# Performance work log

Hardware: AMD Instinct MI355X
Metric: run time of the kernel (lower is better)

The kernel has to match this reference:

```python
import jax, jax.numpy as jnp
import numpy as np

N_NODES = 50000
N_EDGES = 20000
EDGE_SIZE = 32
IN_CH = 256
OUT_CH = 256


def setup_inputs() -> dict:
    key = jax.random.key(0)
    k1, k2, k3 = jax.random.split(key, 3)
    x = jax.random.normal(k1, (N_NODES, IN_CH), dtype=jnp.float32)
    hyperedges = jax.random.randint(k2, (N_EDGES, EDGE_SIZE), 0, N_NODES)
    weight = jax.random.normal(k3, (IN_CH, OUT_CH), dtype=jnp.float32)
    return {"x": x, "hyperedges": hyperedges, "weight": weight}


def reference(x, hyperedges, weight):
    # Gather node features per hyperedge and reduce ('sum' aggregation):
    # [E, K, C] -> [E, C]
    edge_sum = x[hyperedges].sum(axis=1)
    # Scatter-add each hyperedge's summed feature back to every member node.
    agg = jnp.zeros_like(x).at[hyperedges].add(edge_sum[:, None, :])
    # Dense projection + ReLU.
    return jax.nn.relu(agg @ weight)
```

## Files before the change

### kernel.cpp

```cpp
#include <hip/hip_runtime.h>
#include <hip/hip_bf16.h>
#include <hip/hip_fp16.h>

#define N_NODES 50000
#define N_EDGES 20000
#define EDGE_K  32
#define CH      256
#define N_INC   (N_EDGES * EDGE_K)
#define ELL_CAP 64
#define NSLICE  8
#define SCH     32
#define ZROW    N_EDGES

typedef __attribute__((ext_vector_type(4))) float f32x4;
typedef __attribute__((ext_vector_type(8))) _Float16 f16x8;

static __device__ __forceinline__ __half2 u2h2(unsigned int u) {
    __half2 h; __builtin_memcpy(&h, &u, 4); return h;
}
static __device__ __forceinline__ unsigned int h22u(__half2 h) {
    unsigned int u; __builtin_memcpy(&u, &h, 4); return u;
}
static __device__ __forceinline__ unsigned int pk2h(float a, float b) {
    return h22u(__halves2half2(__float2half_rn(a), __float2half_rn(b)));
}

#define CONV_BLOCKS (N_NODES * CH / 8 / 256)
#define ZERO_BLOCKS ((N_NODES + 255) / 256)
#define ELLI_BLOCKS (N_NODES * ELL_CAP / 2 / 256)
__global__ void prep_kernel(const float* __restrict__ x, unsigned short* __restrict__ xb,
                            const float* __restrict__ w, unsigned short* __restrict__ wt,
                            int* __restrict__ deg, unsigned int* __restrict__ ellu,
                            unsigned short* __restrict__ yb) {
    int b = blockIdx.x;
    if (b < CONV_BLOCKS) {
        int i = b * 256 + threadIdx.x;
        int n = i >> 5, sub = i & 31;
        int g = sub >> 2, cp = (sub & 3) * 8;
        const float* src = x + (size_t)n * CH + sub * 8;
        f32x4 v0 = *reinterpret_cast<const f32x4*>(src);
        f32x4 v1 = *reinterpret_cast<const f32x4*>(src + 4);
        uint4 u;
        u.x = pk2h(v0.x, v0.y);
        u.y = pk2h(v0.z, v0.w);
        u.z = pk2h(v1.x, v1.y);
        u.w = pk2h(v1.z, v1.w);
        *reinterpret_cast<uint4*>(xb + ((size_t)g * N_NODES + n) * SCH + cp) = u;
    } else if (b < CONV_BLOCKS + CH) {
        int n = b - CONV_BLOCKS;
        int k = threadIdx.x;
        __half h = __float2half_rn(w[k * CH + n]);
        wt[n * CH + k] = *reinterpret_cast<unsigned short*>(&h);
    } else if (b < CONV_BLOCKS + CH + ZERO_BLOCKS) {
        int i = (b - CONV_BLOCKS - CH) * 256 + threadIdx.x;
        if (i < N_NODES) deg[i] = 0;
    } else if (b < CONV_BLOCKS + CH + ZERO_BLOCKS + ELLI_BLOCKS) {
        int i = (b - CONV_BLOCKS - CH - ZERO_BLOCKS) * 256 + threadIdx.x;
        ellu[i] = 0x4E204E20u;
    } else {
        int g = threadIdx.x >> 5, c = threadIdx.x & 31;
        yb[((size_t)g * (N_EDGES + 1) + ZROW) * SCH + c] = 0;
    }
}

#define FILL_GROUPS   8
#define NODES_PER_GRP (N_NODES / FILL_GROUPS)
#define FILL_WIN      2560
#define FILL_BLOCKS   ((N_INC / FILL_WIN) * FILL_GROUPS)
#define GGRP          (N_EDGES / 16)
#define GATHER_BLOCKS (GGRP * NSLICE)
__global__ __launch_bounds__(256, 4) void gather_fill_kernel(
        const unsigned short* __restrict__ xb, const int* __restrict__ he,
        unsigned short* __restrict__ es, int* __restrict__ deg,
        unsigned short* __restrict__ ell) {
    int b = blockIdx.x;
    if (b < FILL_BLOCKS) {
        int g  = b % FILL_GROUPS;
        int wn = b / FILL_GROUPS;
        int lo = g * NODES_PER_GRP, hi = lo + NODES_PER_GRP;
        int base = wn * FILL_WIN;
#pragma unroll
        for (int it = 0; it < FILL_WIN / 256; ++it) {
            int i = base + it * 256 + threadIdx.x;
            int node = he[i];
            if (node >= lo && node < hi) {
                int slot = atomicAdd(&deg[node], 1);
                if (slot < ELL_CAP)
                    ell[(size_t)node * ELL_CAP + slot] = (unsigned short)(i >> 5);
            }
        }
        return;
    }
    int gb  = b - FILL_BLOCKS;
    int g   = gb & 7;
    int grp = gb >> 3;
    int w = threadIdx.x >> 6, lane = threadIdx.x & 63;
    int ebase = grp * 16 + w * 4;
    const int* hp = he + (size_t)ebase * EDGE_K;
    int s = lane & 15;
    int ep = lane >> 4, k = (lane >> 2) & 3, q = lane & 3;
    int mA = hp[ep * 32 + s];
    int mB = hp[ep * 32 + 16 + s];
    const unsigned short* xg = xb + (size_t)g * N_NODES * SCH;
    int hb = lane & 48;
    int e0 = __shfl(mA, hb + ((0 + k) & 15), 64);
    int e1 = __shfl(mA, hb + ((4 + k) & 15), 64);
    int e2 = __shfl(mA, hb + ((8 + k) & 15), 64);
    int e3 = __shfl(mA, hb + ((12 + k) & 15), 64);
    int e4 = __shfl(mB, hb + ((0 + k) & 15), 64);
    int e5 = __shfl(mB, hb + ((4 + k) & 15), 64);
    int e6 = __shfl(mB, hb + ((8 + k) & 15), 64);
    int e7 = __shfl(mB, hb + ((12 + k) & 15), 64);
    uint4 d0 = *reinterpret_cast<const uint4*>(xg + (size_t)e0 * SCH + q * 8);
    uint4 d1 = *reinterpret_cast<const uint4*>(xg + (size_t)e1 * SCH + q * 8);
    uint4 d2 = *reinterpret_cast<const uint4*>(xg + (size_t)e2 * SCH + q * 8);
    uint4 d3 = *reinterpret_cast<const uint4*>(xg + (size_t)e3 * SCH + q * 8);
    uint4 d4 = *reinterpret_cast<const uint4*>(xg + (size_t)e4 * SCH + q * 8);
    uint4 d5 = *reinterpret_cast<const uint4*>(xg + (size_t)e5 * SCH + q * 8);
    uint4 d6 = *reinterpret_cast<const uint4*>(xg + (size_t)e6 * SCH + q * 8);
    uint4 d7 = *reinterpret_cast<const uint4*>(xg + (size_t)e7 * SCH + q * 8);
    __half2 a0 = u2h2(0u), a1 = u2h2(0u), a2 = u2h2(0u), a3 = u2h2(0u);
    a0 = __hadd2(a0, u2h2(d0.x)); a1 = __hadd2(a1, u2h2(d0.y));
    a2 = __hadd2(a2, u2h2(d0.z)); a3 = __hadd2(a3, u2h2(d0.w));
    a0 = __hadd2(a0, u2h2(d1.x)); a1 = __hadd2(a1, u2h2(d1.y));
    a2 = __hadd2(a2, u2h2(d1.z)); a3 = __hadd2(a3, u2h2(d1.w));
    a0 = __hadd2(a0, u2h2(d2.x)); a1 = __hadd2(a1, u2h2(d2.y));
    a2 = __hadd2(a2, u2h2(d2.z)); a3 = __hadd2(a3, u2h2(d2.w));
    a0 = __hadd2(a0, u2h2(d3.x)); a1 = __hadd2(a1, u2h2(d3.y));
    a2 = __hadd2(a2, u2h2(d3.z)); a3 = __hadd2(a3, u2h2(d3.w));
    a0 = __hadd2(a0, u2h2(d4.x)); a1 = __hadd2(a1, u2h2(d4.y));
    a2 = __hadd2(a2, u2h2(d4.z)); a3 = __hadd2(a3, u2h2(d4.w));
    a0 = __hadd2(a0, u2h2(d5.x)); a1 = __hadd2(a1, u2h2(d5.y));
    a2 = __hadd2(a2, u2h2(d5.z)); a3 = __hadd2(a3, u2h2(d5.w));
    a0 = __hadd2(a0, u2h2(d6.x)); a1 = __hadd2(a1, u2h2(d6.y));
    a2 = __hadd2(a2, u2h2(d6.z)); a3 = __hadd2(a3, u2h2(d6.w));
    a0 = __hadd2(a0, u2h2(d7.x)); a1 = __hadd2(a1, u2h2(d7.y));
    a2 = __hadd2(a2, u2h2(d7.z)); a3 = __hadd2(a3, u2h2(d7.w));
    a0 = __hadd2(a0, u2h2(__shfl_xor(h22u(a0), 4, 64)));
    a1 = __hadd2(a1, u2h2(__shfl_xor(h22u(a1), 4, 64)));
    a2 = __hadd2(a2, u2h2(__shfl_xor(h22u(a2), 4, 64)));
    a3 = __hadd2(a3, u2h2(__shfl_xor(h22u(a3), 4, 64)));
    a0 = __hadd2(a0, u2h2(__shfl_xor(h22u(a0), 8, 64)));
    a1 = __hadd2(a1, u2h2(__shfl_xor(h22u(a1), 8, 64)));
    a2 = __hadd2(a2, u2h2(__shfl_xor(h22u(a2), 8, 64)));
    a3 = __hadd2(a3, u2h2(__shfl_xor(h22u(a3), 8, 64)));
    if ((lane & 12) == 0) {
        uint4 u;
        u.x = h22u(a0); u.y = h22u(a1); u.z = h22u(a2); u.w = h22u(a3);
        *reinterpret_cast<uint4*>(es + (size_t)(ebase + ep) * CH + g * SCH + q * 8) = u;
    }
}

__global__ __launch_bounds__(256) void gemm_kernel(const unsigned short* __restrict__ es,
                                                   const unsigned short* __restrict__ wt,
                                                   unsigned short* __restrict__ yb) {
    int wid  = threadIdx.x >> 6;
    int lane = threadIdx.x & 63;
    int m0   = blockIdx.x * 64 + wid * 16;
    if (m0 >= N_EDGES) return;
    int lr = lane & 15;
    int lg = lane >> 4;

    f32x4 acc[16] = {};
    const unsigned short* arow = es + (size_t)(m0 + lr) * CH + lg * 8;
#pragma unroll
    for (int kk = 0; kk < CH; kk += 32) {
        f16x8 a = *reinterpret_cast<const f16x8*>(arow + kk);
#pragma unroll
        for (int nt = 0; nt < 16; ++nt) {
            f16x8 bb = *reinterpret_cast<const f16x8*>(
                wt + (size_t)(nt * 16 + lr) * CH + kk + lg * 8);
            acc[nt] = __builtin_amdgcn_mfma_f32_16x16x32_f16(a, bb, acc[nt], 0, 0, 0);
        }
    }
#pragma unroll
    for (int nt = 0; nt < 16; ++nt) {
#pragma unroll
        for (int r = 0; r < 4; ++r) {
            int row = m0 + lg * 4 + r;
            __half h = __float2half_rn(acc[nt][r]);
            yb[((size_t)(nt >> 1) * (N_EDGES + 1) + row) * SCH + (nt & 1) * 16 + lr] =
                *reinterpret_cast<unsigned short*>(&h);
        }
    }
}

#define AP_NPB    16
#define AP_BLOCKS ((N_NODES / AP_NPB) * NSLICE)
__global__ __launch_bounds__(256) void apply_kernel(
        const unsigned short* __restrict__ yb, const int* __restrict__ deg,
        const unsigned short* __restrict__ ell, float* __restrict__ out) {
    int b = blockIdx.x;
    int g = b & 7;
    int w = threadIdx.x >> 6, lane = threadIdx.x & 63;
    int np = lane >> 4, s = lane & 15, k = (lane >> 2) & 3, q = lane & 3;
    int node = (b >> 3) * AP_NPB + w * 4 + np;
    int d = deg[node];
    if (d > ELL_CAP) d = ELL_CAP;
    const unsigned short* er = ell + (size_t)node * ELL_CAP;
    int m0 = er[s], m1 = er[16 + s], m2 = er[32 + s], m3 = er[48 + s];
    int dmax = d;
    dmax = max(dmax, __shfl_xor(dmax, 16, 64));
    dmax = max(dmax, __shfl_xor(dmax, 32, 64));
    const unsigned short* yg = yb + (size_t)g * (N_EDGES + 1) * SCH;
    int hb = lane & 48;
    __half2 a0 = u2h2(0u), a1 = u2h2(0u), a2 = u2h2(0u), a3 = u2h2(0u);
    for (int rq = 0; rq < 4; ++rq) {
        if (rq * 16 >= dmax) break;
        int m = (rq == 0) ? m0 : (rq == 1) ? m1 : (rq == 2) ? m2 : m3;
        int e0 = __shfl(m, hb + 0 + k, 64);
        int e1 = __shfl(m, hb + 4 + k, 64);
        int e2 = __shfl(m, hb + 8 + k, 64);
        int e3 = __shfl(m, hb + 12 + k, 64);
        uint4 d0 = *reinterpret_cast<const uint4*>(yg + (size_t)e0 * SCH + q * 8);
        uint4 d1 = *reinterpret_cast<const uint4*>(yg + (size_t)e1 * SCH + q * 8);
        uint4 d2 = *reinterpret_cast<const uint4*>(yg + (size_t)e2 * SCH + q * 8);
        uint4 d3 = *reinterpret_cast<const uint4*>(yg + (size_t)e3 * SCH + q * 8);
        a0 = __hadd2(a0, u2h2(d0.x)); a1 = __hadd2(a1, u2h2(d0.y));
        a2 = __hadd2(a2, u2h2(d0.z)); a3 = __hadd2(a3, u2h2(d0.w));
        a0 = __hadd2(a0, u2h2(d1.x)); a1 = __hadd2(a1, u2h2(d1.y));
        a2 = __hadd2(a2, u2h2(d1.z)); a3 = __hadd2(a3, u2h2(d1.w));
        a0 = __hadd2(a0, u2h2(d2.x)); a1 = __hadd2(a1, u2h2(d2.y));
        a2 = __hadd2(a2, u2h2(d2.z)); a3 = __hadd2(a3, u2h2(d2.w));
        a0 = __hadd2(a0, u2h2(d3.x)); a1 = __hadd2(a1, u2h2(d3.y));
        a2 = __hadd2(a2, u2h2(d3.z)); a3 = __hadd2(a3, u2h2(d3.w));
    }
    a0 = __hadd2(a0, u2h2(__shfl_xor(h22u(a0), 4, 64)));
    a1 = __hadd2(a1, u2h2(__shfl_xor(h22u(a1), 4, 64)));
    a2 = __hadd2(a2, u2h2(__shfl_xor(h22u(a2), 4, 64)));
    a3 = __hadd2(a3, u2h2(__shfl_xor(h22u(a3), 4, 64)));
    a0 = __hadd2(a0, u2h2(__shfl_xor(h22u(a0), 8, 64)));
    a1 = __hadd2(a1, u2h2(__shfl_xor(h22u(a1), 8, 64)));
    a2 = __hadd2(a2, u2h2(__shfl_xor(h22u(a2), 8, 64)));
    a3 = __hadd2(a3, u2h2(__shfl_xor(h22u(a3), 8, 64)));
    if ((lane & 12) == 0) {
        float2 f0 = __half22float2(a0);
        float2 f1 = __half22float2(a1);
        float2 f2 = __half22float2(a2);
        float2 f3 = __half22float2(a3);
        f32x4 r0, r1;
        r0.x = fmaxf(f0.x, 0.f); r0.y = fmaxf(f0.y, 0.f);
        r0.z = fmaxf(f1.x, 0.f); r0.w = fmaxf(f1.y, 0.f);
        r1.x = fmaxf(f2.x, 0.f); r1.y = fmaxf(f2.y, 0.f);
        r1.z = fmaxf(f3.x, 0.f); r1.w = fmaxf(f3.y, 0.f);
        float* dst = out + (size_t)node * CH + g * SCH + q * 8;
        *reinterpret_cast<f32x4*>(dst)     = r0;
        *reinterpret_cast<f32x4*>(dst + 4) = r1;
    }
}

extern "C" void kernel_launch(void* const* d_in, const int* in_sizes, int n_in,
                              void* d_out, int out_size, void* d_ws, size_t ws_size,
                              hipStream_t stream) {
    const float* x  = (const float*)d_in[0];
    const int*   he = (const int*)d_in[1];
    const float* w  = (const float*)d_in[2];
    float* out = (float*)d_out;

    char* ws = (char*)d_ws;
    unsigned short* wt  = (unsigned short*)ws;
    unsigned short* es  = (unsigned short*)(ws + 131072);
    unsigned short* yb  = (unsigned short*)(ws + 10371072);
    int* deg = (int*)(ws + 20611584);
    unsigned short* ell = (unsigned short*)(ws + 20811584);

    unsigned short* xb = (unsigned short*)d_out;

    prep_kernel<<<CONV_BLOCKS + CH + ZERO_BLOCKS + ELLI_BLOCKS + 1, 256, 0, stream>>>(
        x, xb, w, wt, deg, (unsigned int*)ell, yb);

    gather_fill_kernel<<<FILL_BLOCKS + GATHER_BLOCKS, 256, 0, stream>>>(xb, he, es, deg, ell);

    {
        int blocks = (N_EDGES + 63) / 64;
        gemm_kernel<<<blocks, 256, 0, stream>>>(es, wt, yb);
    }

    apply_kernel<<<AP_BLOCKS, 256, 0, stream>>>(yb, deg, ell, out);
}
```

Baseline: 140.9 us.

## Move ELL fill into prep kernel, drop ELL init, unroll apply gather loads

Moves the hyperedge-to-node ELL fill from the gather kernel into the prep kernel and replaces the in-kernel degree zeroing with a memset. The ELL sentinel initialisation is dropped; the apply kernel now masks slots past the node degree to the zero row. The apply kernel issues 8 gather loads up front (16 when needed) instead of a 4-wide loop, and gets a launch bound of 4 blocks per CU. The aim is to cut ELL-init memory traffic, overlap fill atomics with the fp16 conversion, and raise memory-level parallelism in the apply step. This adds one extra memset launch.

```diff
diff --git a/kernel.cpp b/kernel.cpp
--- a/kernel.cpp
+++ b/kernel.cpp
@@ -25,16 +25,33 @@
     return h22u(__halves2half2(__float2half_rn(a), __float2half_rn(b)));
 }
 
-#define CONV_BLOCKS (N_NODES * CH / 8 / 256)
-#define ZERO_BLOCKS ((N_NODES + 255) / 256)
-#define ELLI_BLOCKS (N_NODES * ELL_CAP / 2 / 256)
+#define FILL_GROUPS   8
+#define NODES_PER_GRP (N_NODES / FILL_GROUPS)
+#define FILL_WIN      2560
+#define FILL_BLOCKS   ((N_INC / FILL_WIN) * FILL_GROUPS)
+#define CONV_BLOCKS   (N_NODES * CH / 8 / 256)
 __global__ void prep_kernel(const float* __restrict__ x, unsigned short* __restrict__ xb,
                             const float* __restrict__ w, unsigned short* __restrict__ wt,
-                            int* __restrict__ deg, unsigned int* __restrict__ ellu,
-                            unsigned short* __restrict__ yb) {
+                            const int* __restrict__ he, int* __restrict__ deg,
+                            unsigned short* __restrict__ ell, unsigned short* __restrict__ yb) {
     int b = blockIdx.x;
-    if (b < CONV_BLOCKS) {
-        int i = b * 256 + threadIdx.x;
+    if (b < FILL_BLOCKS) {
+        int g  = b % FILL_GROUPS;
+        int wn = b / FILL_GROUPS;
+        int lo = g * NODES_PER_GRP, hi = lo + NODES_PER_GRP;
+        int base = wn * FILL_WIN;
+#pragma unroll
+        for (int it = 0; it < FILL_WIN / 256; ++it) {
+            int i = base + it * 256 + threadIdx.x;
+            int node = he[i];
+            if (node >= lo && node < hi) {
+                int slot = atomicAdd(&deg[node], 1);
+                if (slot < ELL_CAP)
+                    ell[(size_t)node * ELL_CAP + slot] = (unsigned short)(i >> 5);
+            }
+        }
+    } else if (b < FILL_BLOCKS + CONV_BLOCKS) {
+        int i = (b - FILL_BLOCKS) * 256 + threadIdx.x;
         int n = i >> 5, sub = i & 31;
         int g = sub >> 2, cp = (sub & 3) * 8;
         const float* src = x + (size_t)n * CH + sub * 8;
@@ -46,52 +63,23 @@
         u.z = pk2h(v1.x, v1.y);
         u.w = pk2h(v1.z, v1.w);
         *reinterpret_cast<uint4*>(xb + ((size_t)g * N_NODES + n) * SCH + cp) = u;
-    } else if (b < CONV_BLOCKS + CH) {
-        int n = b - CONV_BLOCKS;
+    } else if (b < FILL_BLOCKS + CONV_BLOCKS + CH) {
+        int n = b - FILL_BLOCKS - CONV_BLOCKS;
         int k = threadIdx.x;
         __half h = __float2half_rn(w[k * CH + n]);
         wt[n * CH + k] = *reinterpret_cast<unsigned short*>(&h);
-    } else if (b < CONV_BLOCKS + CH + ZERO_BLOCKS) {
-        int i = (b - CONV_BLOCKS - CH) * 256 + threadIdx.x;
-        if (i < N_NODES) deg[i] = 0;
-    } else if (b < CONV_BLOCKS + CH + ZERO_BLOCKS + ELLI_BLOCKS) {
-        int i = (b - CONV_BLOCKS - CH - ZERO_BLOCKS) * 256 + threadIdx.x;
-        ellu[i] = 0x4E204E20u;
     } else {
         int g = threadIdx.x >> 5, c = threadIdx.x & 31;
         yb[((size_t)g * (N_EDGES + 1) + ZROW) * SCH + c] = 0;
     }
 }
 
-#define FILL_GROUPS   8
-#define NODES_PER_GRP (N_NODES / FILL_GROUPS)
-#define FILL_WIN      2560
-#define FILL_BLOCKS   ((N_INC / FILL_WIN) * FILL_GROUPS)
 #define GGRP          (N_EDGES / 16)
 #define GATHER_BLOCKS (GGRP * NSLICE)
-__global__ __launch_bounds__(256, 4) void gather_fill_kernel(
+__global__ __launch_bounds__(256, 4) void gather_kernel(
         const unsigned short* __restrict__ xb, const int* __restrict__ he,
-        unsigned short* __restrict__ es, int* __restrict__ deg,
-        unsigned short* __restrict__ ell) {
-    int b = blockIdx.x;
-    if (b < FILL_BLOCKS) {
-        int g  = b % FILL_GROUPS;
-        int wn = b / FILL_GROUPS;
-        int lo = g * NODES_PER_GRP, hi = lo + NODES_PER_GRP;
-        int base = wn * FILL_WIN;
-#pragma unroll
-        for (int it = 0; it < FILL_WIN / 256; ++it) {
-            int i = base + it * 256 + threadIdx.x;
-            int node = he[i];
-            if (node >= lo && node < hi) {
-                int slot = atomicAdd(&deg[node], 1);
-                if (slot < ELL_CAP)
-                    ell[(size_t)node * ELL_CAP + slot] = (unsigned short)(i >> 5);
-            }
-        }
-        return;
-    }
-    int gb  = b - FILL_BLOCKS;
+        unsigned short* __restrict__ es) {
+    int gb  = blockIdx.x;
     int g   = gb & 7;
     int grp = gb >> 3;
     int w = threadIdx.x >> 6, lane = threadIdx.x & 63;
@@ -119,6 +107,7 @@
     uint4 d5 = *reinterpret_cast<const uint4*>(xg + (size_t)e5 * SCH + q * 8);
     uint4 d6 = *reinterpret_cast<const uint4*>(xg + (size_t)e6 * SCH + q * 8);
     uint4 d7 = *reinterpret_cast<const uint4*>(xg + (size_t)e7 * SCH + q * 8);
+    __builtin_amdgcn_sched_barrier(0);
     __half2 a0 = u2h2(0u), a1 = u2h2(0u), a2 = u2h2(0u), a3 = u2h2(0u);
     a0 = __hadd2(a0, u2h2(d0.x)); a1 = __hadd2(a1, u2h2(d0.y));
     a2 = __hadd2(a2, u2h2(d0.z)); a3 = __hadd2(a3, u2h2(d0.w));
@@ -187,7 +176,7 @@
 
 #define AP_NPB    16
 #define AP_BLOCKS ((N_NODES / AP_NPB) * NSLICE)
-__global__ __launch_bounds__(256) void apply_kernel(
+__global__ __launch_bounds__(256, 4) void apply_kernel(
         const unsigned short* __restrict__ yb, const int* __restrict__ deg,
         const unsigned short* __restrict__ ell, float* __restrict__ out) {
     int b = blockIdx.x;
@@ -204,26 +193,73 @@
     dmax = max(dmax, __shfl_xor(dmax, 32, 64));
     const unsigned short* yg = yb + (size_t)g * (N_EDGES + 1) * SCH;
     int hb = lane & 48;
+    int e0 = __shfl(m0, hb + 0 + k, 64);  e0 = (0 + k  < d) ? e0 : ZROW;
+    int e1 = __shfl(m0, hb + 4 + k, 64);  e1 = (4 + k  < d) ? e1 : ZROW;
+    int e2 = __shfl(m0, hb + 8 + k, 64);  e2 = (8 + k  < d) ? e2 : ZROW;
+    int e3 = __shfl(m0, hb + 12 + k, 64); e3 = (12 + k < d) ? e3 : ZROW;
+    int e4 = __shfl(m1, hb + 0 + k, 64);  e4 = (16 + k < d) ? e4 : ZROW;
+    int e5 = __shfl(m1, hb + 4 + k, 64);  e5 = (20 + k < d) ? e5 : ZROW;
+    int e6 = __shfl(m1, hb + 8 + k, 64);  e6 = (24 + k < d) ? e6 : ZROW;
+    int e7 = __shfl(m1, hb + 12 + k, 64); e7 = (28 + k < d) ? e7 : ZROW;
+    uint4 d0 = *reinterpret_cast<const uint4*>(yg + (size_t)e0 * SCH + q * 8);
+    uint4 d1 = *reinterpret_cast<const uint4*>(yg + (size_t)e1 * SCH + q * 8);
+    uint4 d2 = *reinterpret_cast<const uint4*>(yg + (size_t)e2 * SCH + q * 8);
+    uint4 d3 = *reinterpret_cast<const uint4*>(yg + (size_t)e3 * SCH + q * 8);
+    uint4 d4 = *reinterpret_cast<const uint4*>(yg + (size_t)e4 * SCH + q * 8);
+    uint4 d5 = *reinterpret_cast<const uint4*>(yg + (size_t)e5 * SCH + q * 8);
+    uint4 d6 = *reinterpret_cast<const uint4*>(yg + (size_t)e6 * SCH + q * 8);
+    uint4 d7 = *reinterpret_cast<const uint4*>(yg + (size_t)e7 * SCH + q * 8);
+    __builtin_amdgcn_sched_barrier(0);
     __half2 a0 = u2h2(0u), a1 = u2h2(0u), a2 = u2h2(0u), a3 = u2h2(0u);
-    for (int rq = 0; rq < 4; ++rq) {
-        if (rq * 16 >= dmax) break;
-        int m = (rq == 0) ? m0 : (rq == 1) ? m1 : (rq == 2) ? m2 : m3;
-        int e0 = __shfl(m, hb + 0 + k, 64);
-        int e1 = __shfl(m, hb + 4 + k, 64);
-        int e2 = __shfl(m, hb + 8 + k, 64);
-        int e3 = __shfl(m, hb + 12 + k, 64);
-        uint4 d0 = *reinterpret_cast<const uint4*>(yg + (size_t)e0 * SCH + q * 8);
-        uint4 d1 = *reinterpret_cast<const uint4*>(yg + (size_t)e1 * SCH + q * 8);
-        uint4 d2 = *reinterpret_cast<const uint4*>(yg + (size_t)e2 * SCH + q * 8);
-        uint4 d3 = *reinterpret_cast<const uint4*>(yg + (size_t)e3 * SCH + q * 8);
-        a0 = __hadd2(a0, u2h2(d0.x)); a1 = __hadd2(a1, u2h2(d0.y));
-        a2 = __hadd2(a2, u2h2(d0.z)); a3 = __hadd2(a3, u2h2(d0.w));
-        a0 = __hadd2(a0, u2h2(d1.x)); a1 = __hadd2(a1, u2h2(d1.y));
-        a2 = __hadd2(a2, u2h2(d1.z)); a3 = __hadd2(a3, u2h2(d1.w));
-        a0 = __hadd2(a0, u2h2(d2.x)); a1 = __hadd2(a1, u2h2(d2.y));
-        a2 = __hadd2(a2, u2h2(d2.z)); a3 = __hadd2(a3, u2h2(d2.w));
-        a0 = __hadd2(a0, u2h2(d3.x)); a1 = __hadd2(a1, u2h2(d3.y));
-        a2 = __hadd2(a2, u2h2(d3.z)); a3 = __hadd2(a3, u2h2(d3.w));
+    a0 = __hadd2(a0, u2h2(d0.x)); a1 = __hadd2(a1, u2h2(d0.y));
+    a2 = __hadd2(a2, u2h2(d0.z)); a3 = __hadd2(a3, u2h2(d0.w));
+    a0 = __hadd2(a0, u2h2(d1.x)); a1 = __hadd2(a1, u2h2(d1.y));
+    a2 = __hadd2(a2, u2h2(d1.z)); a3 = __hadd2(a3, u2h2(d1.w));
+    a0 = __hadd2(a0, u2h2(d2.x)); a1 = __hadd2(a1, u2h2(d2.y));
+    a2 = __hadd2(a2, u2h2(d2.z)); a3 = __hadd2(a3, u2h2(d2.w));
+    a0 = __hadd2(a0, u2h2(d3.x)); a1 = __hadd2(a1, u2h2(d3.y));
+    a2 = __hadd2(a2, u2h2(d3.z)); a3 = __hadd2(a3, u2h2(d3.w));
+    a0 = __hadd2(a0, u2h2(d4.x)); a1 = __hadd2(a1, u2h2(d4.y));
+    a2 = __hadd2(a2, u2h2(d4.z)); a3 = __hadd2(a3, u2h2(d4.w));
+    a0 = __hadd2(a0, u2h2(d5.x)); a1 = __hadd2(a1, u2h2(d5.y));
+    a2 = __hadd2(a2, u2h2(d5.z)); a3 = __hadd2(a3, u2h2(d5.w));
+    a0 = __hadd2(a0, u2h2(d6.x)); a1 = __hadd2(a1, u2h2(d6.y));
+    a2 = __hadd2(a2, u2h2(d6.z)); a3 = __hadd2(a3, u2h2(d6.w));
+    a0 = __hadd2(a0, u2h2(d7.x)); a1 = __hadd2(a1, u2h2(d7.y));
+    a2 = __hadd2(a2, u2h2(d7.z)); a3 = __hadd2(a3, u2h2(d7.w));
+    if (dmax > 32) {
+        int f0 = __shfl(m2, hb + 0 + k, 64);  f0 = (32 + k < d) ? f0 : ZROW;
+        int f1 = __shfl(m2, hb + 4 + k, 64);  f1 = (36 + k < d) ? f1 : ZROW;
+        int f2 = __shfl(m2, hb + 8 + k, 64);  f2 = (40 + k < d) ? f2 : ZROW;
+        int f3 = __shfl(m2, hb + 12 + k, 64); f3 = (44 + k < d) ? f3 : ZROW;
+        int f4 = __shfl(m3, hb + 0 + k, 64);  f4 = (48 + k < d) ? f4 : ZROW;
+        int f5 = __shfl(m3, hb + 4 + k, 64);  f5 = (52 + k < d) ? f5 : ZROW;
+        int f6 = __shfl(m3, hb + 8 + k, 64);  f6 = (56 + k < d) ? f6 : ZROW;
+        int f7 = __shfl(m3, hb + 12 + k, 64); f7 = (60 + k < d) ? f7 : ZROW;
+        uint4 c0 = *reinterpret_cast<const uint4*>(yg + (size_t)f0 * SCH + q * 8);
+        uint4 c1 = *reinterpret_cast<const uint4*>(yg + (size_t)f1 * SCH + q * 8);
+        uint4 c2 = *reinterpret_cast<const uint4*>(yg + (size_t)f2 * SCH + q * 8);
+        uint4 c3 = *reinterpret_cast<const uint4*>(yg + (size_t)f3 * SCH + q * 8);
+        uint4 c4 = *reinterpret_cast<const uint4*>(yg + (size_t)f4 * SCH + q * 8);
+        uint4 c5 = *reinterpret_cast<const uint4*>(yg + (size_t)f5 * SCH + q * 8);
+        uint4 c6 = *reinterpret_cast<const uint4*>(yg + (size_t)f6 * SCH + q * 8);
+        uint4 c7 = *reinterpret_cast<const uint4*>(yg + (size_t)f7 * SCH + q * 8);
+        a0 = __hadd2(a0, u2h2(c0.x)); a1 = __hadd2(a1, u2h2(c0.y));
+        a2 = __hadd2(a2, u2h2(c0.z)); a3 = __hadd2(a3, u2h2(c0.w));
+        a0 = __hadd2(a0, u2h2(c1.x)); a1 = __hadd2(a1, u2h2(c1.y));
+        a2 = __hadd2(a2, u2h2(c1.z)); a3 = __hadd2(a3, u2h2(c1.w));
+        a0 = __hadd2(a0, u2h2(c2.x)); a1 = __hadd2(a1, u2h2(c2.y));
+        a2 = __hadd2(a2, u2h2(c2.z)); a3 = __hadd2(a3, u2h2(c2.w));
+        a0 = __hadd2(a0, u2h2(c3.x)); a1 = __hadd2(a1, u2h2(c3.y));
+        a2 = __hadd2(a2, u2h2(c3.z)); a3 = __hadd2(a3, u2h2(c3.w));
+        a0 = __hadd2(a0, u2h2(c4.x)); a1 = __hadd2(a1, u2h2(c4.y));
+        a2 = __hadd2(a2, u2h2(c4.z)); a3 = __hadd2(a3, u2h2(c4.w));
+        a0 = __hadd2(a0, u2h2(c5.x)); a1 = __hadd2(a1, u2h2(c5.y));
+        a2 = __hadd2(a2, u2h2(c5.z)); a3 = __hadd2(a3, u2h2(c5.w));
+        a0 = __hadd2(a0, u2h2(c6.x)); a1 = __hadd2(a1, u2h2(c6.y));
+        a2 = __hadd2(a2, u2h2(c6.z)); a3 = __hadd2(a3, u2h2(c6.w));
+        a0 = __hadd2(a0, u2h2(c7.x)); a1 = __hadd2(a1, u2h2(c7.y));
+        a2 = __hadd2(a2, u2h2(c7.z)); a3 = __hadd2(a3, u2h2(c7.w));
     }
     a0 = __hadd2(a0, u2h2(__shfl_xor(h22u(a0), 4, 64)));
     a1 = __hadd2(a1, u2h2(__shfl_xor(h22u(a1), 4, 64)));
@@ -266,10 +302,12 @@
 
     unsigned short* xb = (unsigned short*)d_out;
 
-    prep_kernel<<<CONV_BLOCKS + CH + ZERO_BLOCKS + ELLI_BLOCKS + 1, 256, 0, stream>>>(
-        x, xb, w, wt, deg, (unsigned int*)ell, yb);
-
-    gather_fill_kernel<<<FILL_BLOCKS + GATHER_BLOCKS, 256, 0, stream>>>(xb, he, es, deg, ell);
+    hipMemsetAsync(deg, 0, (size_t)N_NODES * 4, stream);
+
+    prep_kernel<<<FILL_BLOCKS + CONV_BLOCKS + CH + 1, 256, 0, stream>>>(
+        x, xb, w, wt, he, deg, ell, yb);
+
+    gather_kernel<<<GATHER_BLOCKS, 256, 0, stream>>>(xb, he, es);
 
     {
         int blocks = (N_EDGES + 63) / 64;
```

Result: slower. 146.5 us (+4.0%).

## Stage gather rows through LDS with global_load_lds and drop ELL initialization

Applied to the files above, without the earlier changes.

The edge-gather and node-apply kernels now issue their indexed row fetches as direct global-to-LDS loads (global_load_lds), using a rotated sub-chunk layout. Each wave then sums the rows from shared memory, so the loads can all be in flight before any accumulation. The ELL padding init is removed; the apply kernel masks slots past each node's degree to the zero row, and slots beyond 32 are handled by a separate direct-load path. The deg zeroing moves to hipMemsetAsync and the fill window is halved with explicit loads. The 32 KB LDS per block may lower occupancy, and the memset adds an extra launch.

```diff
diff --git a/kernel.cpp b/kernel.cpp
--- a/kernel.cpp
+++ b/kernel.cpp
@@ -25,12 +25,16 @@
     return h22u(__halves2half2(__float2half_rn(a), __float2half_rn(b)));
 }
 
+static __device__ __forceinline__ void gll16(const void* g, void* l) {
+    __builtin_amdgcn_global_load_lds(
+        (const __attribute__((address_space(1))) void*)g,
+        (__attribute__((address_space(3))) void*)l,
+        16, 0, 0);
+}
+
 #define CONV_BLOCKS (N_NODES * CH / 8 / 256)
-#define ZERO_BLOCKS ((N_NODES + 255) / 256)
-#define ELLI_BLOCKS (N_NODES * ELL_CAP / 2 / 256)
 __global__ void prep_kernel(const float* __restrict__ x, unsigned short* __restrict__ xb,
                             const float* __restrict__ w, unsigned short* __restrict__ wt,
-                            int* __restrict__ deg, unsigned int* __restrict__ ellu,
                             unsigned short* __restrict__ yb) {
     int b = blockIdx.x;
     if (b < CONV_BLOCKS) {
@@ -51,12 +55,6 @@
         int k = threadIdx.x;
         __half h = __float2half_rn(w[k * CH + n]);
         wt[n * CH + k] = *reinterpret_cast<unsigned short*>(&h);
-    } else if (b < CONV_BLOCKS + CH + ZERO_BLOCKS) {
-        int i = (b - CONV_BLOCKS - CH) * 256 + threadIdx.x;
-        if (i < N_NODES) deg[i] = 0;
-    } else if (b < CONV_BLOCKS + CH + ZERO_BLOCKS + ELLI_BLOCKS) {
-        int i = (b - CONV_BLOCKS - CH - ZERO_BLOCKS) * 256 + threadIdx.x;
-        ellu[i] = 0x4E204E20u;
     } else {
         int g = threadIdx.x >> 5, c = threadIdx.x & 31;
         yb[((size_t)g * (N_EDGES + 1) + ZROW) * SCH + c] = 0;
@@ -65,30 +63,30 @@
 
 #define FILL_GROUPS   8
 #define NODES_PER_GRP (N_NODES / FILL_GROUPS)
-#define FILL_WIN      2560
+#define FILL_WIN      1280
 #define FILL_BLOCKS   ((N_INC / FILL_WIN) * FILL_GROUPS)
-#define GGRP          (N_EDGES / 16)
-#define GATHER_BLOCKS (GGRP * NSLICE)
-__global__ __launch_bounds__(256, 4) void gather_fill_kernel(
+#define GATHER_BLOCKS ((N_EDGES / 16) * NSLICE)
+__global__ __launch_bounds__(256) void gather_fill_kernel(
         const unsigned short* __restrict__ xb, const int* __restrict__ he,
         unsigned short* __restrict__ es, int* __restrict__ deg,
         unsigned short* __restrict__ ell) {
+    __shared__ __align__(16) unsigned short glds[16384];
     int b = blockIdx.x;
     if (b < FILL_BLOCKS) {
-        int g  = b % FILL_GROUPS;
-        int wn = b / FILL_GROUPS;
+        int g  = b & 7;
+        int wn = b >> 3;
         int lo = g * NODES_PER_GRP, hi = lo + NODES_PER_GRP;
-        int base = wn * FILL_WIN;
-#pragma unroll
-        for (int it = 0; it < FILL_WIN / 256; ++it) {
-            int i = base + it * 256 + threadIdx.x;
-            int node = he[i];
-            if (node >= lo && node < hi) {
-                int slot = atomicAdd(&deg[node], 1);
-                if (slot < ELL_CAP)
-                    ell[(size_t)node * ELL_CAP + slot] = (unsigned short)(i >> 5);
-            }
-        }
+        int i0 = wn * FILL_WIN + threadIdx.x;
+        int n0 = he[i0];
+        int n1 = he[i0 + 256];
+        int n2 = he[i0 + 512];
+        int n3 = he[i0 + 768];
+        int n4 = he[i0 + 1024];
+        if (n0 >= lo && n0 < hi) { int s = atomicAdd(&deg[n0], 1); if (s < ELL_CAP) ell[(size_t)n0 * ELL_CAP + s] = (unsigned short)(i0 >> 5); }
+        if (n1 >= lo && n1 < hi) { int s = atomicAdd(&deg[n1], 1); if (s < ELL_CAP) ell[(size_t)n1 * ELL_CAP + s] = (unsigned short)((i0 + 256) >> 5); }
+        if (n2 >= lo && n2 < hi) { int s = atomicAdd(&deg[n2], 1); if (s < ELL_CAP) ell[(size_t)n2 * ELL_CAP + s] = (unsigned short)((i0 + 512) >> 5); }
+        if (n3 >= lo && n3 < hi) { int s = atomicAdd(&deg[n3], 1); if (s < ELL_CAP) ell[(size_t)n3 * ELL_CAP + s] = (unsigned short)((i0 + 768) >> 5); }
+        if (n4 >= lo && n4 < hi) { int s = atomicAdd(&deg[n4], 1); if (s < ELL_CAP) ell[(size_t)n4 * ELL_CAP + s] = (unsigned short)((i0 + 1024) >> 5); }
         return;
     }
     int gb  = b - FILL_BLOCKS;
@@ -97,45 +95,32 @@
     int w = threadIdx.x >> 6, lane = threadIdx.x & 63;
     int ebase = grp * 16 + w * 4;
     const int* hp = he + (size_t)ebase * EDGE_K;
-    int s = lane & 15;
-    int ep = lane >> 4, k = (lane >> 2) & 3, q = lane & 3;
-    int mA = hp[ep * 32 + s];
-    int mB = hp[ep * 32 + 16 + s];
+    int el = lane >> 4, s = lane & 15;
+    int mA = hp[el * 32 + s];
+    int mB = hp[el * 32 + 16 + s];
     const unsigned short* xg = xb + (size_t)g * N_NODES * SCH;
-    int hb = lane & 48;
-    int e0 = __shfl(mA, hb + ((0 + k) & 15), 64);
-    int e1 = __shfl(mA, hb + ((4 + k) & 15), 64);
-    int e2 = __shfl(mA, hb + ((8 + k) & 15), 64);
-    int e3 = __shfl(mA, hb + ((12 + k) & 15), 64);
-    int e4 = __shfl(mB, hb + ((0 + k) & 15), 64);
-    int e5 = __shfl(mB, hb + ((4 + k) & 15), 64);
-    int e6 = __shfl(mB, hb + ((8 + k) & 15), 64);
-    int e7 = __shfl(mB, hb + ((12 + k) & 15), 64);
-    uint4 d0 = *reinterpret_cast<const uint4*>(xg + (size_t)e0 * SCH + q * 8);
-    uint4 d1 = *reinterpret_cast<const uint4*>(xg + (size_t)e1 * SCH + q * 8);
-    uint4 d2 = *reinterpret_cast<const uint4*>(xg + (size_t)e2 * SCH + q * 8);
-    uint4 d3 = *reinterpret_cast<const uint4*>(xg + (size_t)e3 * SCH + q * 8);
-    uint4 d4 = *reinterpret_cast<const uint4*>(xg + (size_t)e4 * SCH + q * 8);
-    uint4 d5 = *reinterpret_cast<const uint4*>(xg + (size_t)e5 * SCH + q * 8);
-    uint4 d6 = *reinterpret_cast<const uint4*>(xg + (size_t)e6 * SCH + q * 8);
-    uint4 d7 = *reinterpret_cast<const uint4*>(xg + (size_t)e7 * SCH + q * 8);
+    unsigned short* my = &glds[w * 4096];
+    int rsel = lane >> 2;
+    int sub  = (lane + rsel) & 3;
+#pragma unroll
+    for (int t = 0; t < 4; ++t) {
+        int vA = __shfl(mA, t * 16 + rsel, 64);
+        int vB = __shfl(mB, t * 16 + rsel, 64);
+        gll16(xg + (size_t)vA * SCH + sub * 8, my + t * 1024);
+        gll16(xg + (size_t)vB * SCH + sub * 8, my + t * 1024 + 512);
+    }
+    asm volatile("s_waitcnt vmcnt(0)" ::: "memory");
+    __builtin_amdgcn_sched_barrier(0);
+    int t2 = lane >> 4, rr = (lane >> 2) & 3, chunk = lane & 3;
+    int rsub = (chunk - rr) & 3;
+    const unsigned short* rb = my + t2 * 1024 + rr * 32 + rsub * 8;
     __half2 a0 = u2h2(0u), a1 = u2h2(0u), a2 = u2h2(0u), a3 = u2h2(0u);
-    a0 = __hadd2(a0, u2h2(d0.x)); a1 = __hadd2(a1, u2h2(d0.y));
-    a2 = __hadd2(a2, u2h2(d0.z)); a3 = __hadd2(a3, u2h2(d0.w));
-    a0 = __hadd2(a0, u2h2(d1.x)); a1 = __hadd2(a1, u2h2(d1.y));
-    a2 = __hadd2(a2, u2h2(d1.z)); a3 = __hadd2(a3, u2h2(d1.w));
-    a0 = __hadd2(a0, u2h2(d2.x)); a1 = __hadd2(a1, u2h2(d2.y));
-    a2 = __hadd2(a2, u2h2(d2.z)); a3 = __hadd2(a3, u2h2(d2.w));
-    a0 = __hadd2(a0, u2h2(d3.x)); a1 = __hadd2(a1, u2h2(d3.y));
-    a2 = __hadd2(a2, u2h2(d3.z)); a3 = __hadd2(a3, u2h2(d3.w));
-    a0 = __hadd2(a0, u2h2(d4.x)); a1 = __hadd2(a1, u2h2(d4.y));
-    a2 = __hadd2(a2, u2h2(d4.z)); a3 = __hadd2(a3, u2h2(d4.w));
-    a0 = __hadd2(a0, u2h2(d5.x)); a1 = __hadd2(a1, u2h2(d5.y));
-    a2 = __hadd2(a2, u2h2(d5.z)); a3 = __hadd2(a3, u2h2(d5.w));
-    a0 = __hadd2(a0, u2h2(d6.x)); a1 = __hadd2(a1, u2h2(d6.y));
-    a2 = __hadd2(a2, u2h2(d6.z)); a3 = __hadd2(a3, u2h2(d6.w));
-    a0 = __hadd2(a0, u2h2(d7.x)); a1 = __hadd2(a1, u2h2(d7.y));
-    a2 = __hadd2(a2, u2h2(d7.z)); a3 = __hadd2(a3, u2h2(d7.w));
+#pragma unroll
+    for (int i = 0; i < 8; ++i) {
+        uint4 d = *reinterpret_cast<const uint4*>(rb + i * 128);
+        a0 = __hadd2(a0, u2h2(d.x)); a1 = __hadd2(a1, u2h2(d.y));
+        a2 = __hadd2(a2, u2h2(d.z)); a3 = __hadd2(a3, u2h2(d.w));
+    }
     a0 = __hadd2(a0, u2h2(__shfl_xor(h22u(a0), 4, 64)));
     a1 = __hadd2(a1, u2h2(__shfl_xor(h22u(a1), 4, 64)));
     a2 = __hadd2(a2, u2h2(__shfl_xor(h22u(a2), 4, 64)));
@@ -147,7 +132,7 @@
     if ((lane & 12) == 0) {
         uint4 u;
         u.x = h22u(a0); u.y = h22u(a1); u.z = h22u(a2); u.w = h22u(a3);
-        *reinterpret_cast<uint4*>(es + (size_t)(ebase + ep) * CH + g * SCH + q * 8) = u;
+        *reinterpret_cast<uint4*>(es + (size_t)(ebase + t2) * CH + g * SCH + chunk * 8) = u;
     }
 }
 
@@ -185,45 +170,60 @@
     }
 }
 
-#define AP_NPB    16
-#define AP_BLOCKS ((N_NODES / AP_NPB) * NSLICE)
+#define AP_BLOCKS ((N_NODES / 16) * NSLICE)
 __global__ __launch_bounds__(256) void apply_kernel(
         const unsigned short* __restrict__ yb, const int* __restrict__ deg,
         const unsigned short* __restrict__ ell, float* __restrict__ out) {
+    __shared__ __align__(16) unsigned short alds[16384];
     int b = blockIdx.x;
     int g = b & 7;
     int w = threadIdx.x >> 6, lane = threadIdx.x & 63;
-    int np = lane >> 4, s = lane & 15, k = (lane >> 2) & 3, q = lane & 3;
-    int node = (b >> 3) * AP_NPB + w * 4 + np;
-    int d = deg[node];
-    if (d > ELL_CAP) d = ELL_CAP;
-    const unsigned short* er = ell + (size_t)node * ELL_CAP;
-    int m0 = er[s], m1 = er[16 + s], m2 = er[32 + s], m3 = er[48 + s];
-    int dmax = d;
+    int nb = (b >> 3) * 16 + w * 4;
+    int el = lane >> 4, s = lane & 15;
+    int node_own = nb + el;
+    int d_own = deg[node_own];
+    if (d_own > ELL_CAP) d_own = ELL_CAP;
+    const unsigned short* er = ell + (size_t)node_own * ELL_CAP;
+    int m0 = er[s], m1 = er[16 + s];
+    int dmax = d_own;
     dmax = max(dmax, __shfl_xor(dmax, 16, 64));
     dmax = max(dmax, __shfl_xor(dmax, 32, 64));
     const unsigned short* yg = yb + (size_t)g * (N_EDGES + 1) * SCH;
-    int hb = lane & 48;
+    unsigned short* my = &alds[w * 4096];
+    int rsel = lane >> 2;
+    int sub  = (lane + rsel) & 3;
+#pragma unroll
+    for (int t = 0; t < 4; ++t) {
+        int dt = __shfl(d_own, t * 16, 64);
+        int vA = __shfl(m0, t * 16 + rsel, 64); vA = (rsel < dt) ? vA : ZROW;
+        int vB = __shfl(m1, t * 16 + rsel, 64); vB = (16 + rsel < dt) ? vB : ZROW;
+        gll16(yg + (size_t)vA * SCH + sub * 8, my + t * 1024);
+        gll16(yg + (size_t)vB * SCH + sub * 8, my + t * 1024 + 512);
+    }
+    asm volatile("s_waitcnt vmcnt(0)" ::: "memory");
+    __builtin_amdgcn_sched_barrier(0);
+    int t2 = lane >> 4, rr = (lane >> 2) & 3, chunk = lane & 3;
+    int rsub = (chunk - rr) & 3;
+    const unsigned short* rb = my + t2 * 1024 + rr * 32 + rsub * 8;
     __half2 a0 = u2h2(0u), a1 = u2h2(0u), a2 = u2h2(0u), a3 = u2h2(0u);
-    for (int rq = 0; rq < 4; ++rq) {
-        if (rq * 16 >= dmax) break;
-        int m = (rq == 0) ? m0 : (rq == 1) ? m1 : (rq == 2) ? m2 : m3;
-        int e0 = __shfl(m, hb + 0 + k, 64);
-        int e1 = __shfl(m, hb + 4 + k, 64);
-        int e2 = __shfl(m, hb + 8 + k, 64);
-        int e3 = __shfl(m, hb + 12 + k, 64);
-        uint4 d0 = *reinterpret_cast<const uint4*>(yg + (size_t)e0 * SCH + q * 8);
-        uint4 d1 = *reinterpret_cast<const uint4*>(yg + (size_t)e1 * SCH + q * 8);
-        uint4 d2 = *reinterpret_cast<const uint4*>(yg + (size_t)e2 * SCH + q * 8);
-        uint4 d3 = *reinterpret_cast<const uint4*>(yg + (size_t)e3 * SCH + q * 8);
-        a0 = __hadd2(a0, u2h2(d0.x)); a1 = __hadd2(a1, u2h2(d0.y));
-        a2 = __hadd2(a2, u2h2(d0.z)); a3 = __hadd2(a3, u2h2(d0.w));
-        a0 = __hadd2(a0, u2h2(d1.x)); a1 = __hadd2(a1, u2h2(d1.y));
-        a2 = __hadd2(a2, u2h2(d1.z)); a3 = __hadd2(a3, u2h2(d1.w));
-        a0 = __hadd2(a0, u2h2(d2.x)); a1 = __hadd2(a1, u2h2(d2.y));
-        a2 = __hadd2(a2, u2h2(d2.z)); a3 = __hadd2(a3, u2h2(d2.w));
-        a0 = __hadd2(a0, u2h2(d3.x)); a1 = __hadd2(a1, u2h2(d3.y));
-        a2 = __hadd2(a2, u2h2(d3.z)); a3 = __hadd2(a3, u2h2(d3.w));
+#pragma unroll
+    for (int i = 0; i < 8; ++i) {
+        uint4 d = *reinterpret_cast<const uint4*>(rb + i * 128);
+        a0 = __hadd2(a0, u2h2(d.x)); a1 = __hadd2(a1, u2h2(d.y));
+        a2 = __hadd2(a2, u2h2(d.z)); a3 = __hadd2(a3, u2h2(d.w));
+    }
+    if (dmax > 32) {
+        int m2 = er[32 + s], m3 = er[48 + s];
+        int dt2 = __shfl(d_own, t2 * 16, 64);
+#pragma unroll
+        for (int i = 0; i < 8; ++i) {
+            int sl = rr + 4 * i;
+            int v = __shfl((i < 4) ? m2 : m3, t2 * 16 + (sl & 15), 64);
+            v = (32 + sl < dt2) ? v : ZROW;
+            uint4 d = *reinterpret_cast<const uint4*>(yg + (size_t)v * SCH + chunk * 8);
+            a0 = __hadd2(a0, u2h2(d.x)); a1 = __hadd2(a1, u2h2(d.y));
+            a2 = __hadd2(a2, u2h2(d.z)); a3 = __hadd2(a3, u2h2(d.w));
+        }
     }
     a0 = __hadd2(a0, u2h2(__shfl_xor(h22u(a0), 4, 64)));
     a1 = __hadd2(a1, u2h2(__shfl_xor(h22u(a1), 4, 64)));
@@ -234,6 +234,7 @@
     a2 = __hadd2(a2, u2h2(__shfl_xor(h22u(a2), 8, 64)));
     a3 = __hadd2(a3, u2h2(__shfl_xor(h22u(a3), 8, 64)));
     if ((lane & 12) == 0) {
+        int node = nb + t2;
         float2 f0 = __half22float2(a0);
         float2 f1 = __half22float2(a1);
         float2 f2 = __half22float2(a2);
@@ -243,7 +244,7 @@
         r0.z = fmaxf(f1.x, 0.f); r0.w = fmaxf(f1.y, 0.f);
         r1.x = fmaxf(f2.x, 0.f); r1.y = fmaxf(f2.y, 0.f);
         r1.z = fmaxf(f3.x, 0.f); r1.w = fmaxf(f3.y, 0.f);
-        float* dst = out + (size_t)node * CH + g * SCH + q * 8;
+        float* dst = out + (size_t)node * CH + g * SCH + chunk * 8;
         *reinterpret_cast<f32x4*>(dst)     = r0;
         *reinterpret_cast<f32x4*>(dst + 4) = r1;
     }
@@ -266,8 +267,9 @@
 
     unsigned short* xb = (unsigned short*)d_out;
 
-    prep_kernel<<<CONV_BLOCKS + CH + ZERO_BLOCKS + ELLI_BLOCKS + 1, 256, 0, stream>>>(
-        x, xb, w, wt, deg, (unsigned int*)ell, yb);
+    hipMemsetAsync(deg, 0, (size_t)N_NODES * 4, stream);
+
+    prep_kernel<<<CONV_BLOCKS + CH + 1, 256, 0, stream>>>(x, xb, w, wt, yb);
 
     gather_fill_kernel<<<FILL_BLOCKS + GATHER_BLOCKS, 256, 0, stream>>>(xb, he, es, deg, ell);
 
```

Result: slower. 167.7 us (+19.0%).
